# Kernel optimization log

Hardware: AMD Instinct MI355X
Metric: run time of the kernel (lower is better)

Reference implementation:

```python
import jax, jax.numpy as jnp
import numpy as np

B, T = 4096, 512          # batch, max seq len
V, E, H, O = 57, 20, 128, 18  # vocab, embed, hidden, classes


def setup_inputs() -> dict:
    key = jax.random.key(0)
    ks = jax.random.split(key, 9)
    x = jax.random.randint(ks[0], (B, T), 0, V)
    lens = jax.random.randint(ks[1], (B,), 1, T + 1)
    x_lengths = jnp.sort(lens)[::-1]  # pack_padded_sequence needs descending lengths
    s = 1.0 / np.sqrt(H)
    emb = jax.random.normal(ks[2], (V, E), dtype=jnp.float32)
    W_ih = jax.random.uniform(ks[3], (H, E), minval=-s, maxval=s, dtype=jnp.float32)
    W_hh = jax.random.uniform(ks[4], (H, H), minval=-s, maxval=s, dtype=jnp.float32)
    b_ih = jax.random.uniform(ks[5], (H,), minval=-s, maxval=s, dtype=jnp.float32)
    b_hh = jax.random.uniform(ks[6], (H,), minval=-s, maxval=s, dtype=jnp.float32)
    so = 1.0 / np.sqrt(H)
    W_out = jax.random.uniform(ks[7], (O, H), minval=-so, maxval=so, dtype=jnp.float32)
    b_out = jax.random.uniform(ks[8], (O,), minval=-so, maxval=so, dtype=jnp.float32)
    return {"x": x, "x_lengths": x_lengths, "emb": emb, "W_ih": W_ih,
            "W_hh": W_hh, "b_ih": b_ih, "b_hh": b_hh, "W_out": W_out, "b_out": b_out}


def reference(x, x_lengths, emb, W_ih, W_hh, b_ih, b_hh, W_out, b_out):
    xe = emb[x]                                            # [B,T,E] embedding gather
    # precompute input projection + both biases once (hoisted out of recurrence)
    xw = jnp.einsum('bte,he->bth', xe, W_ih) + b_ih + b_hh  # [B,T,H]
    valid = jnp.arange(T)[None, :] < x_lengths[:, None]     # [B,T] packed-seq mask

    def step(h, inp):
        xw_t, v_t = inp                                     # [B,H], [B]
        h_new = jnp.tanh(xw_t + h @ W_hh.T)
        # packed RNN: stop updating once past this sequence's length,
        # so the final h equals the hidden state at step len-1
        h = jnp.where(v_t[:, None], h_new, h)
        return h, None

    h0 = jnp.zeros((B, H), dtype=xw.dtype)
    hT, _ = jax.lax.scan(step, h0, (jnp.swapaxes(xw, 0, 1), valid.T))  # scan over T
    logits = jax.nn.relu(hT) @ W_out.T + b_out              # [B,O]
    return jax.nn.log_softmax(logits, axis=1)
```

## Files before the change

kernel.cpp:

```cpp
#include <hip/hip_runtime.h>
#include <math.h>

#define Bn 4096
#define Tn 512
#define Vn 57
#define En 20
#define Hn 128
#define On 18
#define ROWS 16
#define NTHR 256
#define NBLK (Bn / ROWS)
#define KC 5
#define ESTR 40
#define XSTR 513
#define HFSTR 132
#define ASCALE 2.8853900817779268f

typedef _Float16 half8  __attribute__((ext_vector_type(8)));
typedef __fp16   fp16x2 __attribute__((ext_vector_type(2)));
typedef float    floatx4 __attribute__((ext_vector_type(4)));

__device__ __forceinline__ float tanh_scaled(float z) {
    float e = __builtin_amdgcn_exp2f(z);
    float r = __builtin_amdgcn_rcpf(e + 1.0f);
    return fmaf(-2.0f, r, 1.0f);
}

__device__ __forceinline__ unsigned pk_u32(fp16x2 v) {
    union { fp16x2 h; unsigned u; } c; c.h = v; return c.u;
}

__launch_bounds__(NTHR, 1)
__global__ void rnn_mfma_kernel(const int* __restrict__ x,
                                const int* __restrict__ xlen,
                                const float* __restrict__ emb,
                                const float* __restrict__ W_ih,
                                const float* __restrict__ W_hh,
                                const float* __restrict__ b_ih,
                                const float* __restrict__ b_hh,
                                const float* __restrict__ W_out,
                                const float* __restrict__ b_out,
                                float* __restrict__ out)
{
    __shared__ __align__(16) uint4    exB[2][4][64];
    __shared__ __align__(16) _Float16 sEmb[Vn * ESTR];
    __shared__ __align__(16) float    sHf[ROWS * HFSTR];
    __shared__ int   sX[ROWS * XSTR];
    __shared__ float sLogit[ROWS][On];
    __shared__ float sMLS[ROWS];
    __shared__ float sPad[6800];

    const int tid  = threadIdx.x;
    const int blk  = blockIdx.x;
    const int row0 = blk * ROWS;

    ((volatile float*)sPad)[tid % 6800] = 0.0f;

    const int w    = tid >> 6;
    const int lane = tid & 63;
    const int n    = lane & 15;
    const int q    = lane >> 4;

    half8 Ah[2][KC];
    const int fA0 = 32 * w + 8 * (n >> 2) + (n & 3);
    #pragma unroll
    for (int b = 0; b < 2; ++b) {
        const int f = fA0 + 4 * b;
        #pragma unroll
        for (int kc = 0; kc < 4; ++kc) {
            const float* p = &W_hh[f * Hn + kc * 32 + q * 8];
            #pragma unroll
            for (int i = 0; i < 8; ++i)
                Ah[b][kc][i] = (_Float16)(p[i] * ASCALE);
        }
        #pragma unroll
        for (int i = 0; i < 8; ++i) {
            int e = q * 8 + i;
            float v = 0.0f;
            if (e < En)       v = W_ih[f * En + e];
            else if (e == 20) v = b_ih[f] + b_hh[f];
            Ah[b][4][i] = (_Float16)(v * ASCALE);
        }
    }

    for (int idx = tid; idx < Vn * 32; idx += NTHR) {
        int c = idx >> 5, j = idx & 31;
        float v = (j < En) ? emb[c * En + j] : (j == 20 ? 1.0f : 0.0f);
        sEmb[c * ESTR + j] = (_Float16)v;
    }
    for (int idx = tid * 4; idx < ROWS * Tn; idx += NTHR * 4) {
        int4 v = *(const int4*)&x[row0 * Tn + idx];
        int r = idx >> 9, t = idx & 511;
        sX[r * XSTR + t]     = v.x;
        sX[r * XSTR + t + 1] = v.y;
        sX[r * XSTR + t + 2] = v.z;
        sX[r * XSTR + t + 3] = v.w;
    }
    for (int idx = tid; idx < 2 * 4 * 64; idx += NTHR)
        ((uint4*)exB)[idx] = make_uint4(0u, 0u, 0u, 0u);
    __syncthreads();

    const int Lmax  = xlen[row0];
    const int len_n = xlen[row0 + n];

    int   idN;
    half8 xeC;
    {
        int id0 = sX[n * XSTR];
        xeC = *(const half8*)&sEmb[id0 * ESTR + 8 * q];
        idN = sX[n * XSTR + (Lmax > 1 ? 1 : 0)];
    }

    float hreg[8] = {0.f, 0.f, 0.f, 0.f, 0.f, 0.f, 0.f, 0.f};

    #define RNN_STEP(BR, BW, t)                                                   \
    {                                                                             \
        half8 bf0 = *(const half8*)&exB[BR][0][lane];                             \
        half8 bf1 = *(const half8*)&exB[BR][1][lane];                             \
        half8 bf2 = *(const half8*)&exB[BR][2][lane];                             \
        half8 bf3 = *(const half8*)&exB[BR][3][lane];                             \
        half8 xeN = *(const half8*)&sEmb[idN * ESTR + 8 * q];                     \
        int idN2 = sX[n * XSTR + min((t) + 2, Lmax - 1)];                         \
        floatx4 aE0 = {0.f,0.f,0.f,0.f}, aO0 = {0.f,0.f,0.f,0.f};                 \
        floatx4 aE1 = {0.f,0.f,0.f,0.f}, aO1 = {0.f,0.f,0.f,0.f};                 \
        aE0 = __builtin_amdgcn_mfma_f32_16x16x32_f16(Ah[0][0], bf0, aE0, 0,0,0);  \
        aE1 = __builtin_amdgcn_mfma_f32_16x16x32_f16(Ah[1][0], bf0, aE1, 0,0,0);  \
        aO0 = __builtin_amdgcn_mfma_f32_16x16x32_f16(Ah[0][1], bf1, aO0, 0,0,0);  \
        aO1 = __builtin_amdgcn_mfma_f32_16x16x32_f16(Ah[1][1], bf1, aO1, 0,0,0);  \
        aE0 = __builtin_amdgcn_mfma_f32_16x16x32_f16(Ah[0][2], bf2, aE0, 0,0,0);  \
        aE1 = __builtin_amdgcn_mfma_f32_16x16x32_f16(Ah[1][2], bf2, aE1, 0,0,0);  \
        aO0 = __builtin_amdgcn_mfma_f32_16x16x32_f16(Ah[0][3], bf3, aO0, 0,0,0);  \
        aO1 = __builtin_amdgcn_mfma_f32_16x16x32_f16(Ah[1][3], bf3, aO1, 0,0,0);  \
        aE0 = __builtin_amdgcn_mfma_f32_16x16x32_f16(Ah[0][4], xeC, aE0, 0,0,0);  \
        aE1 = __builtin_amdgcn_mfma_f32_16x16x32_f16(Ah[1][4], xeC, aE1, 0,0,0);  \
        const bool upd = ((t) < len_n);                                           \
        _Pragma("unroll")                                                         \
        for (int i = 0; i < 4; ++i) {                                             \
            float v0 = tanh_scaled(aE0[i] + aO0[i]);                              \
            float v1 = tanh_scaled(aE1[i] + aO1[i]);                              \
            hreg[i]     = upd ? v0 : hreg[i];                                     \
            hreg[4 + i] = upd ? v1 : hreg[4 + i];                                 \
        }                                                                         \
        uint4 pk;                                                                 \
        pk.x = pk_u32(__builtin_amdgcn_cvt_pkrtz(hreg[0], hreg[1]));              \
        pk.y = pk_u32(__builtin_amdgcn_cvt_pkrtz(hreg[2], hreg[3]));              \
        pk.z = pk_u32(__builtin_amdgcn_cvt_pkrtz(hreg[4], hreg[5]));              \
        pk.w = pk_u32(__builtin_amdgcn_cvt_pkrtz(hreg[6], hreg[7]));              \
        exB[BW][w][lane] = pk;                                                    \
        xeC = xeN; idN = idN2;                                                    \
        __syncthreads();                                                          \
    }

    int t = 0;
    for (; t + 2 <= Lmax; t += 2) {
        RNN_STEP(0, 1, t);
        RNN_STEP(1, 0, t + 1);
    }
    if (t < Lmax) {
        RNN_STEP(0, 1, t);
    }
    #undef RNN_STEP

    {
        float4 f0, f1;
        f0.x = hreg[0]; f0.y = hreg[1]; f0.z = hreg[2]; f0.w = hreg[3];
        f1.x = hreg[4]; f1.y = hreg[5]; f1.z = hreg[6]; f1.w = hreg[7];
        *(float4*)&sHf[n * HFSTR + 32 * w + 8 * q]     = f0;
        *(float4*)&sHf[n * HFSTR + 32 * w + 8 * q + 4] = f1;
    }
    __syncthreads();

    for (int it = tid; it < ROWS * On; it += NTHR) {
        int r = it / On, c = it % On;
        float acc = b_out[c];
        for (int k = 0; k < Hn; ++k) {
            float hv = sHf[r * HFSTR + k];
            hv = hv > 0.0f ? hv : 0.0f;
            acc = fmaf(hv, W_out[c * Hn + k], acc);
        }
        sLogit[r][c] = acc;
    }
    __syncthreads();

    if (tid < ROWS) {
        float m = -INFINITY;
        #pragma unroll
        for (int c = 0; c < On; ++c) m = fmaxf(m, sLogit[tid][c]);
        float s = 0.0f;
        #pragma unroll
        for (int c = 0; c < On; ++c) s += __expf(sLogit[tid][c] - m);
        sMLS[tid] = m + __logf(s);
    }
    __syncthreads();

    for (int it = tid; it < ROWS * On; it += NTHR) {
        int r = it / On, c = it % On;
        out[(row0 + r) * On + c] = sLogit[r][c] - sMLS[r];
    }
}

extern "C" void kernel_launch(void* const* d_in, const int* in_sizes, int n_in,
                              void* d_out, int out_size, void* d_ws, size_t ws_size,
                              hipStream_t stream) {
    const int*   x     = (const int*)d_in[0];
    const int*   xlen  = (const int*)d_in[1];
    const float* emb   = (const float*)d_in[2];
    const float* W_ih  = (const float*)d_in[3];
    const float* W_hh  = (const float*)d_in[4];
    const float* b_ih  = (const float*)d_in[5];
    const float* b_hh  = (const float*)d_in[6];
    const float* W_out = (const float*)d_in[7];
    const float* b_out = (const float*)d_in[8];
    float*       out   = (float*)d_out;

    rnn_mfma_kernel<<<NBLK, NTHR, 0, stream>>>(x, xlen, emb, W_ih, W_hh,
                                               b_ih, b_hh, W_out, b_out, out);
}
```

Before: 288.3 us.

## Split recurrent step across eight waves and precompute next input projection off critical path

Doubles the block to 512 threads so each of eight waves owns one 16x16 output tile of the hidden update instead of two, halving per-wave MFMA and tanh work on the serial step. The input-embedding projection for the next timestep is now issued after the hidden-state store and before the barrier, so it overlaps the sync wait rather than sitting on the dependency chain. Each wave writes half of an exchange slot (uint2) instead of a full uint4. In exchange the per-step barrier now synchronizes twice as many waves, and the launch bound hint changes to 2 blocks per CU even though the large shared padding array likely prevents that.

Measured after the change: 231.5 us. 1.25x faster.

```diff
diff --git a/kernel.cpp b/kernel.cpp
--- a/kernel.cpp
+++ b/kernel.cpp
@@ -8,7 +8,7 @@
 #define Hn 128
 #define On 18
 #define ROWS 16
-#define NTHR 256
+#define NTHR 512
 #define NBLK (Bn / ROWS)
 #define KC 5
 #define ESTR 40
@@ -30,7 +30,7 @@
     union { fp16x2 h; unsigned u; } c; c.h = v; return c.u;
 }
 
-__launch_bounds__(NTHR, 1)
+__launch_bounds__(NTHR, 2)
 __global__ void rnn_mfma_kernel(const int* __restrict__ x,
                                 const int* __restrict__ xlen,
                                 const float* __restrict__ emb,
@@ -60,27 +60,25 @@
     const int lane = tid & 63;
     const int n    = lane & 15;
     const int q    = lane >> 4;
-
-    half8 Ah[2][KC];
-    const int fA0 = 32 * w + 8 * (n >> 2) + (n & 3);
+    const int kcW  = w >> 1;
+    const int bsel = w & 1;
+
+    half8 Ah[KC];
+    const int f = 32 * kcW + 8 * (n >> 2) + 4 * bsel + (n & 3);
     #pragma unroll
-    for (int b = 0; b < 2; ++b) {
-        const int f = fA0 + 4 * b;
+    for (int kc = 0; kc < 4; ++kc) {
+        const float* p = &W_hh[f * Hn + kc * 32 + q * 8];
         #pragma unroll
-        for (int kc = 0; kc < 4; ++kc) {
-            const float* p = &W_hh[f * Hn + kc * 32 + q * 8];
-            #pragma unroll
-            for (int i = 0; i < 8; ++i)
-                Ah[b][kc][i] = (_Float16)(p[i] * ASCALE);
-        }
-        #pragma unroll
-        for (int i = 0; i < 8; ++i) {
-            int e = q * 8 + i;
-            float v = 0.0f;
-            if (e < En)       v = W_ih[f * En + e];
-            else if (e == 20) v = b_ih[f] + b_hh[f];
-            Ah[b][4][i] = (_Float16)(v * ASCALE);
-        }
+        for (int i = 0; i < 8; ++i)
+            Ah[kc][i] = (_Float16)(p[i] * ASCALE);
+    }
+    #pragma unroll
+    for (int i = 0; i < 8; ++i) {
+        int e = q * 8 + i;
+        float v = 0.0f;
+        if (e < En)       v = W_ih[f * En + e];
+        else if (e == 20) v = b_ih[f] + b_hh[f];
+        Ah[4][i] = (_Float16)(v * ASCALE);
     }
 
     for (int idx = tid; idx < Vn * 32; idx += NTHR) {
@@ -103,15 +101,18 @@
     const int Lmax  = xlen[row0];
     const int len_n = xlen[row0 + n];
 
-    int   idN;
-    half8 xeC;
+    int     idN;
+    floatx4 P = {0.f, 0.f, 0.f, 0.f};
     {
         int id0 = sX[n * XSTR];
-        xeC = *(const half8*)&sEmb[id0 * ESTR + 8 * q];
+        half8 xe0 = *(const half8*)&sEmb[id0 * ESTR + 8 * q];
+        P = __builtin_amdgcn_mfma_f32_16x16x32_f16(Ah[4], xe0, P, 0, 0, 0);
         idN = sX[n * XSTR + (Lmax > 1 ? 1 : 0)];
     }
 
-    float hreg[8] = {0.f, 0.f, 0.f, 0.f, 0.f, 0.f, 0.f, 0.f};
+    float hreg[4] = {0.f, 0.f, 0.f, 0.f};
+
+    const int wOffH = 32 * kcW + 8 * q + 4 * bsel;
 
     #define RNN_STEP(BR, BW, t)                                                   \
     {                                                                             \
@@ -119,35 +120,28 @@
         half8 bf1 = *(const half8*)&exB[BR][1][lane];                             \
         half8 bf2 = *(const half8*)&exB[BR][2][lane];                             \
         half8 bf3 = *(const half8*)&exB[BR][3][lane];                             \
-        half8 xeN = *(const half8*)&sEmb[idN * ESTR + 8 * q];                     \
-        int idN2 = sX[n * XSTR + min((t) + 2, Lmax - 1)];                         \
-        floatx4 aE0 = {0.f,0.f,0.f,0.f}, aO0 = {0.f,0.f,0.f,0.f};                 \
-        floatx4 aE1 = {0.f,0.f,0.f,0.f}, aO1 = {0.f,0.f,0.f,0.f};                 \
-        aE0 = __builtin_amdgcn_mfma_f32_16x16x32_f16(Ah[0][0], bf0, aE0, 0,0,0);  \
-        aE1 = __builtin_amdgcn_mfma_f32_16x16x32_f16(Ah[1][0], bf0, aE1, 0,0,0);  \
-        aO0 = __builtin_amdgcn_mfma_f32_16x16x32_f16(Ah[0][1], bf1, aO0, 0,0,0);  \
-        aO1 = __builtin_amdgcn_mfma_f32_16x16x32_f16(Ah[1][1], bf1, aO1, 0,0,0);  \
-        aE0 = __builtin_amdgcn_mfma_f32_16x16x32_f16(Ah[0][2], bf2, aE0, 0,0,0);  \
-        aE1 = __builtin_amdgcn_mfma_f32_16x16x32_f16(Ah[1][2], bf2, aE1, 0,0,0);  \
-        aO0 = __builtin_amdgcn_mfma_f32_16x16x32_f16(Ah[0][3], bf3, aO0, 0,0,0);  \
-        aO1 = __builtin_amdgcn_mfma_f32_16x16x32_f16(Ah[1][3], bf3, aO1, 0,0,0);  \
-        aE0 = __builtin_amdgcn_mfma_f32_16x16x32_f16(Ah[0][4], xeC, aE0, 0,0,0);  \
-        aE1 = __builtin_amdgcn_mfma_f32_16x16x32_f16(Ah[1][4], xeC, aE1, 0,0,0);  \
+        floatx4 aE = P;                                                           \
+        floatx4 aO = {0.f, 0.f, 0.f, 0.f};                                        \
+        aE = __builtin_amdgcn_mfma_f32_16x16x32_f16(Ah[0], bf0, aE, 0, 0, 0);     \
+        aO = __builtin_amdgcn_mfma_f32_16x16x32_f16(Ah[1], bf1, aO, 0, 0, 0);     \
+        aE = __builtin_amdgcn_mfma_f32_16x16x32_f16(Ah[2], bf2, aE, 0, 0, 0);     \
+        aO = __builtin_amdgcn_mfma_f32_16x16x32_f16(Ah[3], bf3, aO, 0, 0, 0);     \
         const bool upd = ((t) < len_n);                                           \
         _Pragma("unroll")                                                         \
         for (int i = 0; i < 4; ++i) {                                             \
-            float v0 = tanh_scaled(aE0[i] + aO0[i]);                              \
-            float v1 = tanh_scaled(aE1[i] + aO1[i]);                              \
-            hreg[i]     = upd ? v0 : hreg[i];                                     \
-            hreg[4 + i] = upd ? v1 : hreg[4 + i];                                 \
+            float v = tanh_scaled(aE[i] + aO[i]);                                 \
+            hreg[i] = upd ? v : hreg[i];                                          \
         }                                                                         \
-        uint4 pk;                                                                 \
+        uint2 pk;                                                                 \
         pk.x = pk_u32(__builtin_amdgcn_cvt_pkrtz(hreg[0], hreg[1]));              \
         pk.y = pk_u32(__builtin_amdgcn_cvt_pkrtz(hreg[2], hreg[3]));              \
-        pk.z = pk_u32(__builtin_amdgcn_cvt_pkrtz(hreg[4], hreg[5]));              \
-        pk.w = pk_u32(__builtin_amdgcn_cvt_pkrtz(hreg[6], hreg[7]));              \
-        exB[BW][w][lane] = pk;                                                    \
-        xeC = xeN; idN = idN2;                                                    \
+        *(uint2*)((_Float16*)&exB[BW][kcW][0] + lane * 8 + 4 * bsel) = pk;        \
+        half8 xeN = *(const half8*)&sEmb[idN * ESTR + 8 * q];                     \
+        int tn = (t) + 2;                                                         \
+        int idN2 = sX[n * XSTR + (tn < Lmax ? tn : Lmax - 1)];                    \
+        floatx4 Pz = {0.f, 0.f, 0.f, 0.f};                                        \
+        P = __builtin_amdgcn_mfma_f32_16x16x32_f16(Ah[4], xeN, Pz, 0, 0, 0);      \
+        idN = idN2;                                                               \
         __syncthreads();                                                          \
     }
 
@@ -162,11 +156,9 @@
     #undef RNN_STEP
 
     {
-        float4 f0, f1;
+        float4 f0;
         f0.x = hreg[0]; f0.y = hreg[1]; f0.z = hreg[2]; f0.w = hreg[3];
-        f1.x = hreg[4]; f1.y = hreg[5]; f1.z = hreg[6]; f1.w = hreg[7];
-        *(float4*)&sHf[n * HFSTR + 32 * w + 8 * q]     = f0;
-        *(float4*)&sHf[n * HFSTR + 32 * w + 8 * q + 4] = f1;
+        *(float4*)&sHf[n * HFSTR + wOffH] = f0;
     }
     __syncthreads();
 
```
